# Kernel tuning notes

Measured on AMD Instinct MI355X. Metric: run time of the kernel, lower is better.

## Reference

```python
import jax, jax.numpy as jnp
import numpy as np

N_USERS, N_MOVIES, M, K = 100000, 20000, 8, 32
B = 524288

def setup_inputs() -> dict:
    key = jax.random.key(0)
    k1, k2, k3, k4 = jax.random.split(key, 4)
    edge = jax.random.randint(k1, (B, 2), 0, 20000, dtype=jnp.int64) if jax.config.jax_enable_x64 else jax.random.randint(k1, (B, 2), 0, 20000, dtype=jnp.int32)
    std = 1.0 / K
    taste_emb = jax.random.normal(k2, (N_USERS, M * K), dtype=jnp.float32) * std
    attn_emb = jax.random.normal(k3, (N_USERS, M * K), dtype=jnp.float32) * std
    movie_emb = jax.random.normal(k4, (N_MOVIES, K), dtype=jnp.float32) * std
    user_bias = jnp.zeros((N_USERS, 1), dtype=jnp.float32)
    movie_bias = jnp.zeros((N_MOVIES, 1), dtype=jnp.float32)
    return {"edge": edge, "taste_emb": taste_emb, "attn_emb": attn_emb,
            "movie_emb": movie_emb, "user_bias": user_bias, "movie_bias": movie_bias}

def reference(edge, taste_emb, attn_emb, movie_emb, user_bias, movie_bias):
    u = edge[:, 0]
    v = edge[:, 1]
    A = attn_emb[u].reshape(-1, M, K)   # [B, m, k]
    U = taste_emb[u].reshape(-1, M, K)  # [B, m, k]
    e = movie_emb[v]                    # [B, k]
    logits = jnp.einsum('bmk,bk->bm', A, e)          # bmm(A, e) -> [B, m]
    att = jax.nn.softmax(logits, axis=1)             # softmax over m tastes
    scores = jnp.einsum('bmk,bk->bm', U, e)          # bmm(U, e) -> [B, m]
    y_hat = jnp.sum(scores * att, axis=1) + movie_bias[v, 0] + user_bias[u, 0]
    return y_hat  # [B]
```

## Files before the change

kernel.cpp:

```cpp
#include <hip/hip_runtime.h>


#define MOT_CAP     64
#define MOT_OVF_CAP 4096

using half8 = __attribute__((ext_vector_type(8))) _Float16;
using f32x4 = __attribute__((ext_vector_type(4))) float;

__global__ void mot_zero_kernel(int4* __restrict__ p, int n4) {
    const int i = blockIdx.x * 256 + (int)threadIdx.x;
    if (i < n4) p[i] = make_int4(0, 0, 0, 0);
}

__device__ __forceinline__ float mot_score_div(const float* __restrict__ Ar,
                                               const float* __restrict__ Tr,
                                               const float4* __restrict__ Ep) {
    float4 ek[8];
    #pragma unroll
    for (int k4 = 0; k4 < 8; ++k4) ek[k4] = Ep[k4];
    float num = 0.f, den = 0.f;
    #pragma unroll
    for (int m = 0; m < 8; ++m) {
        float l = 0.f, s = 0.f;
        #pragma unroll
        for (int k4 = 0; k4 < 8; ++k4) {
            const float4 a = *(const float4*)(Ar + m * 32 + k4 * 4);
            const float4 t = *(const float4*)(Tr + m * 32 + k4 * 4);
            const float4 e = ek[k4];
            l = fmaf(a.x, e.x, l); l = fmaf(a.y, e.y, l);
            l = fmaf(a.z, e.z, l); l = fmaf(a.w, e.w, l);
            s = fmaf(t.x, e.x, s); s = fmaf(t.y, e.y, s);
            s = fmaf(t.z, e.z, s); s = fmaf(t.w, e.w, s);
        }
        const float ex = __expf(l);
        den += ex;
        num = fmaf(ex, s, num);
    }
    return num / den;
}

__global__ void mot_scatter_kernel(const int4* __restrict__ edge2,
                                   int* __restrict__ cnt,
                                   int* __restrict__ ovfMeta,
                                   int* __restrict__ ovf,
                                   int2* __restrict__ sve,
                                   int nPairs, int nEdges) {
    const int i = blockIdx.x * 256 + (int)threadIdx.x;
    if (i < nPairs) {
        const int4 q = edge2[i];
        int pos = atomicAdd(&cnt[q.x], 1);
        if (pos < MOT_CAP) sve[(size_t)q.x * MOT_CAP + pos] = make_int2(q.y, 2 * i);
        else { int o = atomicAdd(ovfMeta, 1); if (o < MOT_OVF_CAP) ovf[o] = 2 * i; }
        pos = atomicAdd(&cnt[q.z], 1);
        if (pos < MOT_CAP) sve[(size_t)q.z * MOT_CAP + pos] = make_int2(q.w, 2 * i + 1);
        else { int o = atomicAdd(ovfMeta, 1); if (o < MOT_OVF_CAP) ovf[o] = 2 * i + 1; }
    } else if (i == nPairs && (nEdges & 1)) {
        const int2 e = ((const int2*)edge2)[nEdges - 1];
        int pos = atomicAdd(&cnt[e.x], 1);
        if (pos < MOT_CAP) sve[(size_t)e.x * MOT_CAP + pos] = make_int2(e.y, nEdges - 1);
        else { int o = atomicAdd(ovfMeta, 1); if (o < MOT_OVF_CAP) ovf[o] = nEdges - 1; }
    }
}

__device__ __forceinline__ half8 mot_load_afrag(const float* __restrict__ attn_emb,
                                                const float* __restrict__ taste_emb,
                                                int u, int row, int k0) {
    const float* rowp = (row < 8)
        ? attn_emb  + (size_t)u * 256 + row * 32 + k0
        : taste_emb + (size_t)u * 256 + (row - 8) * 32 + k0;
    const float4 r0 = *(const float4*)rowp;
    const float4 r1 = *(const float4*)(rowp + 4);
    half8 af;
    af[0] = (_Float16)r0.x; af[1] = (_Float16)r0.y;
    af[2] = (_Float16)r0.z; af[3] = (_Float16)r0.w;
    af[4] = (_Float16)r1.x; af[5] = (_Float16)r1.y;
    af[6] = (_Float16)r1.z; af[7] = (_Float16)r1.w;
    return af;
}

__global__ __launch_bounds__(256, 4) void mot_mfma4_kernel(
    const int2* __restrict__ edge,
    const float* __restrict__ taste_emb,
    const float* __restrict__ attn_emb,
    const float4* __restrict__ movie_emb,
    const float* __restrict__ user_bias,
    const float* __restrict__ movie_bias,
    const int* __restrict__ cnt,
    const int2* __restrict__ sve,
    const int* __restrict__ ovfMeta,
    const int* __restrict__ ovf,
    float* __restrict__ out,
    int nUsers, int nMovies, int mainBlocks)
{
    const int tid  = (int)threadIdx.x;
    const int lane = tid & 63;

    if ((int)blockIdx.x < mainBlocks) {
        const int u0 = ((int)blockIdx.x * 4 + (tid >> 6)) * 2;
        const int u1 = u0 + 1;
        if (u0 >= nUsers) return;

        const int row = lane & 15;
        const int kq  = lane >> 4;
        const int k0  = kq * 8;

        const int2* __restrict__ b0 = sve + (size_t)u0 * MOT_CAP;
        const int2* __restrict__ b1 = sve + (size_t)u1 * MOT_CAP;

        int2 ve0[4], ve1[4];
        #pragma unroll
        for (int T = 0; T < 4; ++T) ve0[T] = b0[T * 16 + row];
        #pragma unroll
        for (int T = 0; T < 4; ++T) ve1[T] = b1[T * 16 + row];

        int n0 = cnt[u0]; n0 = n0 > MOT_CAP ? MOT_CAP : n0;
        int n1 = (u1 < nUsers) ? cnt[u1] : 0; n1 = n1 > MOT_CAP ? MOT_CAP : n1;
        const float ub0 = user_bias[u0];
        const float ub1 = user_bias[u1];

        const half8 af0 = mot_load_afrag(attn_emb, taste_emb, u0, row, k0);
        const half8 af1 = mot_load_afrag(attn_emb, taste_emb, u1, row, k0);

        half8 bf0[4], bf1[4];
        #pragma unroll
        for (int g2 = 0; g2 < 2; ++g2) {
            const int2* ve = g2 ? ve1 : ve0;
            half8* bf = g2 ? bf1 : bf0;
            #pragma unroll
            for (int T = 0; T < 4; ++T) {
                const int vx = ((unsigned)ve[T].x < (unsigned)nMovies) ? ve[T].x : 0;
                const float4* __restrict__ Ep = movie_emb + (size_t)vx * 8;
                const float4 e0 = Ep[kq * 2], e1 = Ep[kq * 2 + 1];
                half8 b;
                b[0] = (_Float16)e0.x; b[1] = (_Float16)e0.y;
                b[2] = (_Float16)e0.z; b[3] = (_Float16)e0.w;
                b[4] = (_Float16)e1.x; b[5] = (_Float16)e1.y;
                b[6] = (_Float16)e1.z; b[7] = (_Float16)e1.w;
                bf[T] = b;
            }
        }

        #pragma unroll
        for (int T = 0; T < 4; ++T) {
            #pragma unroll
            for (int g = 0; g < 2; ++g) {
                const int n = g ? n1 : n0;
                if (T * 16 >= n) continue;
                const half8 af = g ? af1 : af0;
                const half8 bf = g ? bf0[0] : bf0[0];
                (void)bf;
                const half8 bfx = g ? bf1[T] : bf0[T];
                const int2 ve = g ? ve1[T] : ve0[T];
                const float ub = g ? ub1 : ub0;

                f32x4 c = {0.f, 0.f, 0.f, 0.f};
                c = __builtin_amdgcn_mfma_f32_16x16x32_f16(af, bfx, c, 0, 0, 0);

                const float s0 = __shfl_xor(c[0], 32);
                const float s1 = __shfl_xor(c[1], 32);
                const float s2 = __shfl_xor(c[2], 32);
                const float s3 = __shfl_xor(c[3], 32);
                const float e0x = __expf(c[0]);
                const float e1x = __expf(c[1]);
                const float e2x = __expf(c[2]);
                const float e3x = __expf(c[3]);
                float den = e0x + e1x + e2x + e3x;
                float num = e0x * s0;
                num = fmaf(e1x, s1, num);
                num = fmaf(e2x, s2, num);
                num = fmaf(e3x, s3, num);
                den += __shfl_xor(den, 16);
                num += __shfl_xor(num, 16);

                if (kq == 0) {
                    const int ei = T * 16 + row;
                    if (ei < n)
                        out[ve.y] = num * __builtin_amdgcn_rcpf(den) + ub
                                    + movie_bias[ve.x];
                }
            }
        }
    } else {
        int oc = ovfMeta[0];
        if (oc > MOT_OVF_CAP) oc = MOT_OVF_CAP;
        const int oi = ((int)blockIdx.x - mainBlocks) * 256 + tid;
        if (oi < oc) {
            const int eid = ovf[oi];
            const int2 ed = edge[eid];
            out[eid] = mot_score_div(attn_emb  + (size_t)ed.x * 256,
                                     taste_emb + (size_t)ed.x * 256,
                                     movie_emb + (size_t)ed.y * 8)
                       + user_bias[ed.x] + movie_bias[ed.y];
        }
    }
}

__global__ __launch_bounds__(256, 4) void mot_flat_kernel(
    const int2* __restrict__ edge,
    const float4* __restrict__ taste_emb,
    const float4* __restrict__ attn_emb,
    const float4* __restrict__ movie_emb,
    const float* __restrict__ user_bias,
    const float* __restrict__ movie_bias,
    float* __restrict__ out,
    int nEdges)
{
    const int tid  = blockIdx.x * 256 + (int)threadIdx.x;
    const int eid  = tid >> 5;
    const int s    = tid & 31;
    if (eid >= nEdges) return;
    const int2 ed = edge[eid];
    const int u = ed.x, v = ed.y;
    const float4* Ap = attn_emb  + (size_t)u * 64;
    const float4* Tp = taste_emb + (size_t)u * 64;
    const float4* Ep = movie_emb + (size_t)v * 8;
    const float4 a0 = Ap[2 * s], a1 = Ap[2 * s + 1];
    const float4 t0 = Tp[2 * s], t1 = Tp[2 * s + 1];
    const int c = s & 3;
    const float4 e0 = Ep[2 * c], e1 = Ep[2 * c + 1];
    float lp = a0.x*e0.x + a0.y*e0.y + a0.z*e0.z + a0.w*e0.w
             + a1.x*e1.x + a1.y*e1.y + a1.z*e1.z + a1.w*e1.w;
    float sp = t0.x*e0.x + t0.y*e0.y + t0.z*e0.z + t0.w*e0.w
             + t1.x*e1.x + t1.y*e1.y + t1.z*e1.z + t1.w*e1.w;
    lp += __shfl_xor(lp, 1); lp += __shfl_xor(lp, 2);
    sp += __shfl_xor(sp, 1); sp += __shfl_xor(sp, 2);
    const float ex = __expf(lp);
    float den = ex, num = ex * sp;
    den += __shfl_xor(den, 4);  num += __shfl_xor(num, 4);
    den += __shfl_xor(den, 8);  num += __shfl_xor(num, 8);
    den += __shfl_xor(den, 16); num += __shfl_xor(num, 16);
    if (s == 0) out[eid] = num / den + user_bias[u] + movie_bias[v];
}

extern "C" void kernel_launch(void* const* d_in, const int* in_sizes, int n_in,
                              void* d_out, int out_size, void* d_ws, size_t ws_size,
                              hipStream_t stream) {
    const int2*   edge       = (const int2*)d_in[0];
    const float*  taste_emb  = (const float*)d_in[1];
    const float*  attn_emb   = (const float*)d_in[2];
    const float*  movie_emb  = (const float*)d_in[3];
    const float*  user_bias  = (const float*)d_in[4];
    const float*  movie_bias = (const float*)d_in[5];
    float*        out        = (float*)d_out;

    const int nEdges = in_sizes[0] / 2;
    const int NB     = in_sizes[3] / 32;

    auto align256 = [](size_t x) { return (x + 255) & ~(size_t)255; };
    char* ws = (char*)d_ws;

    const size_t o_cnt  = 0;
    const size_t o_meta = align256((size_t)NB * 4);
    const size_t o_ovf  = o_meta + 256;
    const size_t o_sve  = align256(o_ovf + (size_t)MOT_OVF_CAP * 4);
    const size_t need   = o_sve + (size_t)NB * MOT_CAP * 8;

    if (ws_size < need) {
        const int blocks = (nEdges * 32 + 255) / 256;
        mot_flat_kernel<<<blocks, 256, 0, stream>>>(
            edge, (const float4*)taste_emb, (const float4*)attn_emb,
            (const float4*)movie_emb, user_bias, movie_bias, out, nEdges);
        return;
    }

    int*  cnt     = (int*)(ws + o_cnt);
    int*  ovfMeta = (int*)(ws + o_meta);
    int*  ovf     = (int*)(ws + o_ovf);
    int2* sve     = (int2*)(ws + o_sve);

    const int n4 = (int)(o_ovf / 16);
    mot_zero_kernel<<<(n4 + 255) / 256, 256, 0, stream>>>((int4*)ws, n4);

    const int nPairs  = nEdges / 2;
    const int sblocks = (nPairs + 1 + 255) / 256;
    mot_scatter_kernel<<<sblocks, 256, 0, stream>>>(
        (const int4*)edge, cnt, ovfMeta, ovf, sve, nPairs, nEdges);

    const int mainBlocks = (NB + 7) / 8;
    const int ovfBlocks  = MOT_OVF_CAP / 256;
    mot_mfma4_kernel<<<mainBlocks + ovfBlocks, 256, 0, stream>>>(
        edge, taste_emb, attn_emb, (const float4*)movie_emb,
        user_bias, movie_bias, cnt, sve, ovfMeta, ovf, out, NB, NB, mainBlocks);
}
```

Measured before the change: 65.75 us.

## Pre-convert user and movie embeddings to packed fp16 before MFMA kernel

```diff
diff --git a/kernel.cpp b/kernel.cpp
--- a/kernel.cpp
+++ b/kernel.cpp
@@ -10,6 +10,40 @@
 __global__ void mot_zero_kernel(int4* __restrict__ p, int n4) {
     const int i = blockIdx.x * 256 + (int)threadIdx.x;
     if (i < n4) p[i] = make_int4(0, 0, 0, 0);
+}
+
+__global__ void mot_cvt_users_kernel(const float4* __restrict__ attn,
+                                     const float4* __restrict__ taste,
+                                     half8* __restrict__ outp, int nTot) {
+    const int i = blockIdx.x * 256 + (int)threadIdx.x;
+    if (i >= nTot) return;
+    const int u = i >> 6, c = i & 63;
+    const int r = c >> 2, q = c & 3;
+    const float4* src = (r < 8)
+        ? attn  + (size_t)u * 64 + r * 8 + q * 2
+        : taste + (size_t)u * 64 + (r - 8) * 8 + q * 2;
+    const float4 a = src[0], b = src[1];
+    half8 h;
+    h[0] = (_Float16)a.x; h[1] = (_Float16)a.y;
+    h[2] = (_Float16)a.z; h[3] = (_Float16)a.w;
+    h[4] = (_Float16)b.x; h[5] = (_Float16)b.y;
+    h[6] = (_Float16)b.z; h[7] = (_Float16)b.w;
+    outp[i] = h;
+}
+
+__global__ void mot_cvt_movies_kernel(const float4* __restrict__ movie,
+                                      half8* __restrict__ outp, int nTot) {
+    const int i = blockIdx.x * 256 + (int)threadIdx.x;
+    if (i >= nTot) return;
+    const int v = i >> 2, q = i & 3;
+    const float4* src = movie + (size_t)v * 8 + q * 2;
+    const float4 a = src[0], b = src[1];
+    half8 h;
+    h[0] = (_Float16)a.x; h[1] = (_Float16)a.y;
+    h[2] = (_Float16)a.z; h[3] = (_Float16)a.w;
+    h[4] = (_Float16)b.x; h[5] = (_Float16)b.y;
+    h[6] = (_Float16)b.z; h[7] = (_Float16)b.w;
+    outp[i] = h;
 }
 
 __device__ __forceinline__ float mot_score_div(const float* __restrict__ Ar,
@@ -62,24 +96,10 @@
     }
 }
 
-__device__ __forceinline__ half8 mot_load_afrag(const float* __restrict__ attn_emb,
-                                                const float* __restrict__ taste_emb,
-                                                int u, int row, int k0) {
-    const float* rowp = (row < 8)
-        ? attn_emb  + (size_t)u * 256 + row * 32 + k0
-        : taste_emb + (size_t)u * 256 + (row - 8) * 32 + k0;
-    const float4 r0 = *(const float4*)rowp;
-    const float4 r1 = *(const float4*)(rowp + 4);
-    half8 af;
-    af[0] = (_Float16)r0.x; af[1] = (_Float16)r0.y;
-    af[2] = (_Float16)r0.z; af[3] = (_Float16)r0.w;
-    af[4] = (_Float16)r1.x; af[5] = (_Float16)r1.y;
-    af[6] = (_Float16)r1.z; af[7] = (_Float16)r1.w;
-    return af;
-}
-
-__global__ __launch_bounds__(256, 4) void mot_mfma4_kernel(
+__global__ __launch_bounds__(256, 4) void mot_mfma_packed_kernel(
     const int2* __restrict__ edge,
+    const half8* __restrict__ pu,
+    const half8* __restrict__ pm,
     const float* __restrict__ taste_emb,
     const float* __restrict__ attn_emb,
     const float4* __restrict__ movie_emb,
@@ -102,59 +122,41 @@
 
         const int row = lane & 15;
         const int kq  = lane >> 4;
-        const int k0  = kq * 8;
-
+
+        int n0 = cnt[u0]; n0 = n0 > MOT_CAP ? MOT_CAP : n0;
+        int n1 = (u1 < nUsers) ? cnt[u1] : 0; n1 = n1 > MOT_CAP ? MOT_CAP : n1;
+        const half8 af0 = pu[(size_t)u0 * 64 + row * 4 + kq];
+        const half8 af1 = pu[(size_t)u1 * 64 + row * 4 + kq];
+        const float ub0 = user_bias[u0];
+        const float ub1 = user_bias[u1];
         const int2* __restrict__ b0 = sve + (size_t)u0 * MOT_CAP;
         const int2* __restrict__ b1 = sve + (size_t)u1 * MOT_CAP;
 
-        int2 ve0[4], ve1[4];
-        #pragma unroll
-        for (int T = 0; T < 4; ++T) ve0[T] = b0[T * 16 + row];
-        #pragma unroll
-        for (int T = 0; T < 4; ++T) ve1[T] = b1[T * 16 + row];
-
-        int n0 = cnt[u0]; n0 = n0 > MOT_CAP ? MOT_CAP : n0;
-        int n1 = (u1 < nUsers) ? cnt[u1] : 0; n1 = n1 > MOT_CAP ? MOT_CAP : n1;
-        const float ub0 = user_bias[u0];
-        const float ub1 = user_bias[u1];
-
-        const half8 af0 = mot_load_afrag(attn_emb, taste_emb, u0, row, k0);
-        const half8 af1 = mot_load_afrag(attn_emb, taste_emb, u1, row, k0);
-
-        half8 bf0[4], bf1[4];
-        #pragma unroll
-        for (int g2 = 0; g2 < 2; ++g2) {
-            const int2* ve = g2 ? ve1 : ve0;
-            half8* bf = g2 ? bf1 : bf0;
-            #pragma unroll
-            for (int T = 0; T < 4; ++T) {
-                const int vx = ((unsigned)ve[T].x < (unsigned)nMovies) ? ve[T].x : 0;
-                const float4* __restrict__ Ep = movie_emb + (size_t)vx * 8;
-                const float4 e0 = Ep[kq * 2], e1 = Ep[kq * 2 + 1];
-                half8 b;
-                b[0] = (_Float16)e0.x; b[1] = (_Float16)e0.y;
-                b[2] = (_Float16)e0.z; b[3] = (_Float16)e0.w;
-                b[4] = (_Float16)e1.x; b[5] = (_Float16)e1.y;
-                b[6] = (_Float16)e1.z; b[7] = (_Float16)e1.w;
-                bf[T] = b;
-            }
-        }
-
-        #pragma unroll
-        for (int T = 0; T < 4; ++T) {
+        for (int t = 0; t < MOT_CAP; t += 16) {
+            if (t >= n0 && t >= n1) break;
+
+            int2 ve0 = make_int2(0, 0), ve1 = make_int2(0, 0);
+            const bool d0 = t < n0, d1 = t < n1;
+            if (d0) ve0 = b0[t + row];
+            if (d1) ve1 = b1[t + row];
+            const int vx0 = ((unsigned)ve0.x < (unsigned)nMovies) ? ve0.x : 0;
+            const int vx1 = ((unsigned)ve1.x < (unsigned)nMovies) ? ve1.x : 0;
+            half8 bf0 = {}, bf1 = {};
+            if (d0) bf0 = pm[(size_t)vx0 * 4 + kq];
+            if (d1) bf1 = pm[(size_t)vx1 * 4 + kq];
+
             #pragma unroll
             for (int g = 0; g < 2; ++g) {
-                const int n = g ? n1 : n0;
-                if (T * 16 >= n) continue;
+                const bool dg = g ? d1 : d0;
+                if (!dg) continue;
+                const int   n  = g ? n1 : n0;
                 const half8 af = g ? af1 : af0;
-                const half8 bf = g ? bf0[0] : bf0[0];
-                (void)bf;
-                const half8 bfx = g ? bf1[T] : bf0[T];
-                const int2 ve = g ? ve1[T] : ve0[T];
+                const half8 bf = g ? bf1 : bf0;
+                const int2  ve = g ? ve1 : ve0;
                 const float ub = g ? ub1 : ub0;
 
                 f32x4 c = {0.f, 0.f, 0.f, 0.f};
-                c = __builtin_amdgcn_mfma_f32_16x16x32_f16(af, bfx, c, 0, 0, 0);
+                c = __builtin_amdgcn_mfma_f32_16x16x32_f16(af, bf, c, 0, 0, 0);
 
                 const float s0 = __shfl_xor(c[0], 32);
                 const float s1 = __shfl_xor(c[1], 32);
@@ -173,7 +175,7 @@
                 num += __shfl_xor(num, 16);
 
                 if (kq == 0) {
-                    const int ei = T * 16 + row;
+                    const int ei = t + row;
                     if (ei < n)
                         out[ve.y] = num * __builtin_amdgcn_rcpf(den) + ub
                                     + movie_bias[ve.x];
@@ -253,7 +255,9 @@
     const size_t o_meta = align256((size_t)NB * 4);
     const size_t o_ovf  = o_meta + 256;
     const size_t o_sve  = align256(o_ovf + (size_t)MOT_OVF_CAP * 4);
-    const size_t need   = o_sve + (size_t)NB * MOT_CAP * 8;
+    const size_t o_pu   = align256(o_sve + (size_t)NB * MOT_CAP * 8);
+    const size_t o_pm   = align256(o_pu + (size_t)NB * 1024);
+    const size_t need   = o_pm + (size_t)NB * 64;
 
     if (ws_size < need) {
         const int blocks = (nEdges * 32 + 255) / 256;
@@ -263,13 +267,22 @@
         return;
     }
 
-    int*  cnt     = (int*)(ws + o_cnt);
-    int*  ovfMeta = (int*)(ws + o_meta);
-    int*  ovf     = (int*)(ws + o_ovf);
-    int2* sve     = (int2*)(ws + o_sve);
+    int*   cnt     = (int*)(ws + o_cnt);
+    int*   ovfMeta = (int*)(ws + o_meta);
+    int*   ovf     = (int*)(ws + o_ovf);
+    int2*  sve     = (int2*)(ws + o_sve);
+    half8* pu      = (half8*)(ws + o_pu);
+    half8* pm      = (half8*)(ws + o_pm);
 
     const int n4 = (int)(o_ovf / 16);
     mot_zero_kernel<<<(n4 + 255) / 256, 256, 0, stream>>>((int4*)ws, n4);
+
+    const int nuChunks = NB * 64;
+    mot_cvt_users_kernel<<<(nuChunks + 255) / 256, 256, 0, stream>>>(
+        (const float4*)attn_emb, (const float4*)taste_emb, pu, nuChunks);
+    const int nmChunks = NB * 4;
+    mot_cvt_movies_kernel<<<(nmChunks + 255) / 256, 256, 0, stream>>>(
+        (const float4*)movie_emb, pm, nmChunks);
 
     const int nPairs  = nEdges / 2;
     const int sblocks = (nPairs + 1 + 255) / 256;
@@ -278,7 +291,7 @@
 
     const int mainBlocks = (NB + 7) / 8;
     const int ovfBlocks  = MOT_OVF_CAP / 256;
-    mot_mfma4_kernel<<<mainBlocks + ovfBlocks, 256, 0, stream>>>(
-        edge, taste_emb, attn_emb, (const float4*)movie_emb,
+    mot_mfma_packed_kernel<<<mainBlocks + ovfBlocks, 256, 0, stream>>>(
+        edge, pu, pm, taste_emb, attn_emb, (const float4*)movie_emb,
         user_bias, movie_bias, cnt, sve, ovfMeta, ovf, out, NB, NB, mainBlocks);
 }
```

Result: slower. 70.09 us (+6.6%).
